# Performance work log

Hardware: AMD Instinct MI355X
Metric: run time of the kernel (lower is better)

## Reference

```python
import jax, jax.numpy as jnp
import numpy as np

D = 256  # channel dim and CBP output dim


def setup_inputs() -> dict:
    key = jax.random.key(0)
    ks = jax.random.split(key, 14)
    B, C, H, W = 32, 256, 56, 56
    attr_num = 400
    inp = {}
    inp["entity_feature"] = jax.random.normal(ks[0], (B, C, H, W), jnp.float32)
    inp["attr_one_hot"] = jax.random.uniform(ks[1], (B, attr_num), jnp.float32)
    # textual_emb: Linear(attr_num, 256)
    inp["W_emb"] = jax.random.normal(ks[2], (D, attr_num), jnp.float32) * 0.02
    inp["b_emb"] = jnp.zeros((D,), jnp.float32)
    # conv: Conv2d(256,256,1)
    inp["conv_w"] = jax.random.normal(ks[3], (D, D), jnp.float32) * 0.02
    inp["conv_b"] = jnp.zeros((D,), jnp.float32)
    # mcb_conv1_attr: Conv2d(256,32,1)
    inp["conv1_w"] = jax.random.normal(ks[4], (32, D), jnp.float32) * 0.05
    inp["conv1_b"] = jnp.zeros((32,), jnp.float32)
    # mcb_conv2_attr: Conv2d(32,1,1)
    inp["conv2_w"] = jax.random.normal(ks[5], (1, 32), jnp.float32) * 0.1
    inp["conv2_b"] = jnp.zeros((1,), jnp.float32)
    # CompactBilinearPooling count-sketch tables (fixed random at init)
    inp["h1"] = jax.random.randint(ks[6], (D,), 0, D, jnp.int32)
    inp["h2"] = jax.random.randint(ks[7], (D,), 0, D, jnp.int32)
    inp["s1"] = (jax.random.randint(ks[8], (D,), 0, 2, jnp.int32) * 2 - 1).astype(jnp.float32)
    inp["s2"] = (jax.random.randint(ks[9], (D,), 0, 2, jnp.int32) * 2 - 1).astype(jnp.float32)
    return inp


def _sketch_matrix(h, s):
    # sparse count-sketch projection as dense [C_in, D] matrix: P[i, h[i]] = s[i]
    return jnp.zeros((D, D), jnp.float32).at[jnp.arange(D), h].add(s)


def reference(entity_feature, attr_one_hot, W_emb, b_emb, conv_w, conv_b,
              conv1_w, conv1_b, conv2_w, conv2_b, h1, h2, s1, s2):
    feature = jax.nn.relu(entity_feature)                      # [B,256,H,W]
    # textual embedding + spatially-constant 1x1 conv (identical math to
    # expanding then convolving, since the expanded tensor is constant over HxW)
    t = attr_one_hot @ W_emb.T + b_emb                         # [B,256]
    a = t @ conv_w.T + conv_b                                  # [B,256]

    # Compact Bilinear Pooling (count sketch -> FFT -> elementwise mul -> iFFT)
    P1 = _sketch_matrix(h1, s1)
    P2 = _sketch_matrix(h2, s2)
    sk1 = a @ P1                                               # [B,256], spatially constant
    sk2 = jnp.einsum('bchw,cd->bdhw', feature, P2)             # [B,256,H,W]
    fft1 = jnp.fft.rfft(sk1, n=D, axis=1)[:, :, None, None]    # [B,129,1,1]
    fft2 = jnp.fft.rfft(sk2, n=D, axis=1)                      # [B,129,H,W]
    mcb = jnp.fft.irfft(fft1 * fft2, n=D, axis=1)              # [B,256,H,W]

    # gating chain: conv1x1 -> relu -> conv1x1 -> sigmoid
    x = jax.nn.relu(jnp.einsum('bchw,oc->bohw', mcb, conv1_w) + conv1_b[None, :, None, None])
    attr_map = jax.nn.sigmoid(jnp.einsum('bchw,oc->bohw', x, conv2_w) + conv2_b[None, :, None, None])  # [B,1,H,W]
    attr_feature = attr_map * entity_feature                   # [B,256,H,W]
    return attr_map, attr_feature
```

## Files before the change

kernel.cpp:

```cpp
#include <hip/hip_runtime.h>

#define Dq    256
#define ATTR  400
#define HW    3136
#define NB    32
#define PXT   64
#define NTILE 49

typedef __attribute__((ext_vector_type(8))) short bf16x8;
typedef __attribute__((ext_vector_type(4))) float f32x4;

__device__ __forceinline__ unsigned short f2bf(float f) {
  unsigned int x = __float_as_uint(f);
  return (unsigned short)((x + 0x7FFFu + ((x >> 16) & 1u)) >> 16);
}

__device__ __forceinline__ void g2lds16(const float* g, float* l) {
  __builtin_amdgcn_global_load_lds(
      (const __attribute__((address_space(1))) unsigned int*)g,
      (__attribute__((address_space(3))) unsigned int*)l,
      16, 0, 0);
}

__global__ __launch_bounds__(256) void k_sk1(
    const float* __restrict__ oh, const float* __restrict__ W_emb,
    const float* __restrict__ b_emb, const float* __restrict__ conv_w,
    const float* __restrict__ conv_b, const int* __restrict__ h1,
    const float* __restrict__ s1, float* __restrict__ sk1_out) {
  __shared__ float ohs[ATTR];
  __shared__ float ts[Dq];
  __shared__ float sk[Dq];
  const int b = blockIdx.x, tid = threadIdx.x;
  for (int j = tid; j < ATTR; j += 256) ohs[j] = oh[b * ATTR + j];
  sk[tid] = 0.f;
  __syncthreads();
  float acc = b_emb[tid];
  const float* wr = W_emb + tid * ATTR;
  for (int j = 0; j < ATTR; ++j) acc = fmaf(ohs[j], wr[j], acc);
  ts[tid] = acc;
  __syncthreads();
  float a = conv_b[tid];
  const float* cr = conv_w + tid * Dq;
  for (int k = 0; k < Dq; ++k) a = fmaf(ts[k], cr[k], a);
  atomicAdd(&sk[h1[tid]], a * s1[tid]);
  __syncthreads();
  sk1_out[b * Dq + tid] = sk[tid];
}

__global__ __launch_bounds__(256) void k_G(
    const float* __restrict__ sk1, const float* __restrict__ conv1_w,
    const int* __restrict__ h2, const float* __restrict__ s2,
    unsigned short* __restrict__ Abuf) {
  __shared__ float sks[Dq];
  __shared__ float w1[Dq];
  __shared__ float Tl[Dq];
  const int b = blockIdx.x >> 5, o = blockIdx.x & 31, c = threadIdx.x;
  sks[c] = sk1[b * Dq + c];
  w1[c]  = conv1_w[o * Dq + c];
  __syncthreads();
  float t = 0.f;
  for (int d = 0; d < Dq; ++d) t = fmaf(w1[d], sks[(d - c) & 255], t);
  Tl[c] = t;
  __syncthreads();
  const float g = s2[c] * Tl[h2[c]];
  const int frag = (o >> 4) * 8 + (c >> 5);
  const int lane = (o & 15) | (((c >> 3) & 3) << 4);
  Abuf[(((size_t)b * 16 + frag) * 64 + lane) * 8 + (c & 7)] = f2bf(g);
}

__global__ __launch_bounds__(256) void k_tile(
    const float* __restrict__ ent,
    const unsigned short* __restrict__ Abuf,
    const float* __restrict__ c1b, const float* __restrict__ c2w,
    const float* __restrict__ c2b,
    float* __restrict__ out)
{
  __shared__ float tile[Dq * PXT];
  __shared__ float s_lds[PXT];
  const int b = blockIdx.y;
  const int px_base = blockIdx.x * PXT;
  const int t = threadIdx.x;
  const int w = t >> 6, l = t & 63;

  const float* eb = ent + (size_t)b * Dq * HW + px_base;

#pragma unroll
  for (int i = 0; i < 16; ++i) {
    const int cb = w * 64 + i * 4;
    const float* src = eb + (size_t)(cb + (l >> 4)) * HW + 4 * (l & 15);
    g2lds16(src, &tile[cb * PXT]);
  }
  asm volatile("s_waitcnt vmcnt(0)");
  __syncthreads();

  const int n = l & 15, kg = l >> 4;
  const unsigned short* Ab = Abuf + ((size_t)b * 16 * 64 + l) * 8;

  f32x4 acc0 = {0.f, 0.f, 0.f, 0.f}, acc1 = {0.f, 0.f, 0.f, 0.f};
#pragma unroll
  for (int ks = 0; ks < 8; ++ks) {
    bf16x8 bv;
#pragma unroll
    for (int j = 0; j < 8; ++j) {
      const float fv = tile[(ks * 32 + kg * 8 + j) * PXT + w * 16 + n];
      bv[j] = (short)f2bf(fmaxf(fv, 0.f));
    }
    bf16x8 a0 = *reinterpret_cast<const bf16x8*>(Ab + (size_t)(0 * 8 + ks) * 64 * 8);
    bf16x8 a1 = *reinterpret_cast<const bf16x8*>(Ab + (size_t)(1 * 8 + ks) * 64 * 8);
    acc0 = __builtin_amdgcn_mfma_f32_16x16x32_bf16(a0, bv, acc0, 0, 0, 0);
    acc1 = __builtin_amdgcn_mfma_f32_16x16x32_bf16(a1, bv, acc1, 0, 0, 0);
  }

  const float4 b1a = reinterpret_cast<const float4*>(c1b)[kg];
  const float4 b1b = reinterpret_cast<const float4*>(c1b)[kg + 4];
  const float4 w2a = reinterpret_cast<const float4*>(c2w)[kg];
  const float4 w2b = reinterpret_cast<const float4*>(c2w)[kg + 4];
  float z = 0.f;
  z = fmaf(w2a.x, fmaxf(acc0[0] + b1a.x, 0.f), z);
  z = fmaf(w2a.y, fmaxf(acc0[1] + b1a.y, 0.f), z);
  z = fmaf(w2a.z, fmaxf(acc0[2] + b1a.z, 0.f), z);
  z = fmaf(w2a.w, fmaxf(acc0[3] + b1a.w, 0.f), z);
  z = fmaf(w2b.x, fmaxf(acc1[0] + b1b.x, 0.f), z);
  z = fmaf(w2b.y, fmaxf(acc1[1] + b1b.y, 0.f), z);
  z = fmaf(w2b.z, fmaxf(acc1[2] + b1b.z, 0.f), z);
  z = fmaf(w2b.w, fmaxf(acc1[3] + b1b.w, 0.f), z);
  z += __shfl_xor(z, 16);
  z += __shfl_xor(z, 32);
  const float s = 1.f / (1.f + __expf(-(z + c2b[0])));
  if (l < 16) {
    out[(size_t)b * HW + px_base + w * 16 + l] = s;
    s_lds[w * 16 + l] = s;
  }
  __syncthreads();

  const f32x4 s4v = *reinterpret_cast<const f32x4*>(&s_lds[(t & 15) * 4]);
  float* fb = out + (size_t)NB * HW + (size_t)b * Dq * HW + px_base;
#pragma unroll
  for (int k = 0; k < 16; ++k) {
    const int c = k * 16 + (t >> 4);
    f32x4 e = *reinterpret_cast<const f32x4*>(&tile[c * PXT + (t & 15) * 4]);
    *reinterpret_cast<f32x4*>(fb + (size_t)c * HW + (t & 15) * 4) = e * s4v;
  }
}

extern "C" void kernel_launch(void* const* d_in, const int* in_sizes, int n_in,
                              void* d_out, int out_size, void* d_ws, size_t ws_size,
                              hipStream_t stream) {
  const float* ent    = (const float*)d_in[0];
  const float* oh     = (const float*)d_in[1];
  const float* W_emb  = (const float*)d_in[2];
  const float* b_emb  = (const float*)d_in[3];
  const float* conv_w = (const float*)d_in[4];
  const float* conv_b = (const float*)d_in[5];
  const float* c1w    = (const float*)d_in[6];
  const float* c1b    = (const float*)d_in[7];
  const float* c2w    = (const float*)d_in[8];
  const float* c2b    = (const float*)d_in[9];
  const int*   h1     = (const int*)d_in[10];
  const int*   h2     = (const int*)d_in[11];
  const float* s1     = (const float*)d_in[12];
  const float* s2     = (const float*)d_in[13];

  float* ws  = (float*)d_ws;
  float* sk1 = ws;
  unsigned short* Abuf = (unsigned short*)(ws + NB * Dq);

  hipLaunchKernelGGL(k_sk1, dim3(NB), dim3(256), 0, stream,
                     oh, W_emb, b_emb, conv_w, conv_b, h1, s1, sk1);
  hipLaunchKernelGGL(k_G, dim3(NB * 32), dim3(256), 0, stream,
                     sk1, c1w, h2, s2, Abuf);
  hipLaunchKernelGGL(k_tile, dim3(NTILE, NB), dim3(256), 0, stream,
                     ent, Abuf, c1b, c2w, c2b, (float*)d_out);
}
```

Measured before the change: 73.22 us.

## Make tile kernel persistent with double-buffered LDS prefetch of entity tiles

The tile kernel becomes persistent: 256 blocks loop over all 1568 batch×pixel tiles instead of one tile per block. Each block keeps two 64 KB LDS tile buffers and issues global-to-LDS loads for the next tile before computing the current one, synchronising with vmcnt waits and raw barriers. The aim is to hide the streaming load latency behind the MFMA gating and output writes, and to cut block launch overhead. In exchange, the 128 KB LDS footprint limits each CU to one 4-wave block, so much less latency is hidden by occupancy. The vmcnt waits also cover outstanding stores, which can stall the loop.

```diff
diff --git a/kernel.cpp b/kernel.cpp
--- a/kernel.cpp
+++ b/kernel.cpp
@@ -5,7 +5,7 @@
 #define HW    3136
 #define NB    32
 #define PXT   64
-#define NTILE 49
+#define NTT   (NB * 49)
 
 typedef __attribute__((ext_vector_type(8))) short bf16x8;
 typedef __attribute__((ext_vector_type(4))) float f32x4;
@@ -75,71 +75,94 @@
     const float* __restrict__ c2b,
     float* __restrict__ out)
 {
-  __shared__ float tile[Dq * PXT];
+  __shared__ float tile[2][Dq * PXT];
   __shared__ float s_lds[PXT];
-  const int b = blockIdx.y;
-  const int px_base = blockIdx.x * PXT;
   const int t = threadIdx.x;
   const int w = t >> 6, l = t & 63;
-
-  const float* eb = ent + (size_t)b * Dq * HW + px_base;
-
-#pragma unroll
-  for (int i = 0; i < 16; ++i) {
-    const int cb = w * 64 + i * 4;
-    const float* src = eb + (size_t)(cb + (l >> 4)) * HW + 4 * (l & 15);
-    g2lds16(src, &tile[cb * PXT]);
-  }
-  asm volatile("s_waitcnt vmcnt(0)");
-  __syncthreads();
-
   const int n = l & 15, kg = l >> 4;
-  const unsigned short* Ab = Abuf + ((size_t)b * 16 * 64 + l) * 8;
-
-  f32x4 acc0 = {0.f, 0.f, 0.f, 0.f}, acc1 = {0.f, 0.f, 0.f, 0.f};
-#pragma unroll
-  for (int ks = 0; ks < 8; ++ks) {
-    bf16x8 bv;
-#pragma unroll
-    for (int j = 0; j < 8; ++j) {
-      const float fv = tile[(ks * 32 + kg * 8 + j) * PXT + w * 16 + n];
-      bv[j] = (short)f2bf(fmaxf(fv, 0.f));
-    }
-    bf16x8 a0 = *reinterpret_cast<const bf16x8*>(Ab + (size_t)(0 * 8 + ks) * 64 * 8);
-    bf16x8 a1 = *reinterpret_cast<const bf16x8*>(Ab + (size_t)(1 * 8 + ks) * 64 * 8);
-    acc0 = __builtin_amdgcn_mfma_f32_16x16x32_bf16(a0, bv, acc0, 0, 0, 0);
-    acc1 = __builtin_amdgcn_mfma_f32_16x16x32_bf16(a1, bv, acc1, 0, 0, 0);
-  }
 
   const float4 b1a = reinterpret_cast<const float4*>(c1b)[kg];
   const float4 b1b = reinterpret_cast<const float4*>(c1b)[kg + 4];
   const float4 w2a = reinterpret_cast<const float4*>(c2w)[kg];
   const float4 w2b = reinterpret_cast<const float4*>(c2w)[kg + 4];
-  float z = 0.f;
-  z = fmaf(w2a.x, fmaxf(acc0[0] + b1a.x, 0.f), z);
-  z = fmaf(w2a.y, fmaxf(acc0[1] + b1a.y, 0.f), z);
-  z = fmaf(w2a.z, fmaxf(acc0[2] + b1a.z, 0.f), z);
-  z = fmaf(w2a.w, fmaxf(acc0[3] + b1a.w, 0.f), z);
-  z = fmaf(w2b.x, fmaxf(acc1[0] + b1b.x, 0.f), z);
-  z = fmaf(w2b.y, fmaxf(acc1[1] + b1b.y, 0.f), z);
-  z = fmaf(w2b.z, fmaxf(acc1[2] + b1b.z, 0.f), z);
-  z = fmaf(w2b.w, fmaxf(acc1[3] + b1b.w, 0.f), z);
-  z += __shfl_xor(z, 16);
-  z += __shfl_xor(z, 32);
-  const float s = 1.f / (1.f + __expf(-(z + c2b[0])));
-  if (l < 16) {
-    out[(size_t)b * HW + px_base + w * 16 + l] = s;
-    s_lds[w * 16 + l] = s;
+  const float c2b0 = c2b[0];
+
+  {
+    const int ti = blockIdx.x;
+    const int bb = ti / 49, pxt = ti - bb * 49;
+    const float* eb = ent + (size_t)bb * Dq * HW + pxt * PXT;
+#pragma unroll
+    for (int i = 0; i < 16; ++i) {
+      const int cb = w * 64 + i * 4;
+      g2lds16(eb + (size_t)(cb + (l >> 4)) * HW + 4 * (l & 15), &tile[0][cb * PXT]);
+    }
   }
-  __syncthreads();
 
-  const f32x4 s4v = *reinterpret_cast<const f32x4*>(&s_lds[(t & 15) * 4]);
-  float* fb = out + (size_t)NB * HW + (size_t)b * Dq * HW + px_base;
+  int buf = 0;
+  for (int ti = blockIdx.x; ti < NTT; ti += 256, buf ^= 1) {
+    const int nxt = ti + 256;
+    if (nxt < NTT) {
+      const int bb = nxt / 49, pxt = nxt - bb * 49;
+      const float* eb = ent + (size_t)bb * Dq * HW + pxt * PXT;
 #pragma unroll
-  for (int k = 0; k < 16; ++k) {
-    const int c = k * 16 + (t >> 4);
-    f32x4 e = *reinterpret_cast<const f32x4*>(&tile[c * PXT + (t & 15) * 4]);
-    *reinterpret_cast<f32x4*>(fb + (size_t)c * HW + (t & 15) * 4) = e * s4v;
+      for (int i = 0; i < 16; ++i) {
+        const int cb = w * 64 + i * 4;
+        g2lds16(eb + (size_t)(cb + (l >> 4)) * HW + 4 * (l & 15), &tile[buf ^ 1][cb * PXT]);
+      }
+    }
+    asm volatile("s_waitcnt vmcnt(16)" ::: "memory");
+    __builtin_amdgcn_sched_barrier(0);
+    __builtin_amdgcn_s_barrier();
+
+    const int bb = ti / 49, pxt = ti - bb * 49;
+    const int px_base = pxt * PXT;
+    const float* tb = &tile[buf][0];
+
+    const unsigned short* Ab = Abuf + ((size_t)bb * 16 * 64 + l) * 8;
+    f32x4 acc0 = {0.f, 0.f, 0.f, 0.f}, acc1 = {0.f, 0.f, 0.f, 0.f};
+#pragma unroll
+    for (int ks = 0; ks < 8; ++ks) {
+      bf16x8 bv;
+#pragma unroll
+      for (int j = 0; j < 8; ++j) {
+        const float fv = tb[(ks * 32 + kg * 8 + j) * PXT + w * 16 + n];
+        bv[j] = (short)f2bf(fmaxf(fv, 0.f));
+      }
+      bf16x8 a0 = *reinterpret_cast<const bf16x8*>(Ab + (size_t)(0 * 8 + ks) * 64 * 8);
+      bf16x8 a1 = *reinterpret_cast<const bf16x8*>(Ab + (size_t)(1 * 8 + ks) * 64 * 8);
+      acc0 = __builtin_amdgcn_mfma_f32_16x16x32_bf16(a0, bv, acc0, 0, 0, 0);
+      acc1 = __builtin_amdgcn_mfma_f32_16x16x32_bf16(a1, bv, acc1, 0, 0, 0);
+    }
+
+    float z = 0.f;
+    z = fmaf(w2a.x, fmaxf(acc0[0] + b1a.x, 0.f), z);
+    z = fmaf(w2a.y, fmaxf(acc0[1] + b1a.y, 0.f), z);
+    z = fmaf(w2a.z, fmaxf(acc0[2] + b1a.z, 0.f), z);
+    z = fmaf(w2a.w, fmaxf(acc0[3] + b1a.w, 0.f), z);
+    z = fmaf(w2b.x, fmaxf(acc1[0] + b1b.x, 0.f), z);
+    z = fmaf(w2b.y, fmaxf(acc1[1] + b1b.y, 0.f), z);
+    z = fmaf(w2b.z, fmaxf(acc1[2] + b1b.z, 0.f), z);
+    z = fmaf(w2b.w, fmaxf(acc1[3] + b1b.w, 0.f), z);
+    z += __shfl_xor(z, 16);
+    z += __shfl_xor(z, 32);
+    const float s = 1.f / (1.f + __expf(-(z + c2b0)));
+    if (l < 16) {
+      out[(size_t)bb * HW + px_base + w * 16 + l] = s;
+      s_lds[w * 16 + l] = s;
+    }
+    asm volatile("s_waitcnt lgkmcnt(0)" ::: "memory");
+    __builtin_amdgcn_s_barrier();
+
+    const f32x4 s4v = *reinterpret_cast<const f32x4*>(&s_lds[(t & 15) * 4]);
+    float* fb = out + (size_t)NB * HW + (size_t)bb * Dq * HW + px_base;
+#pragma unroll
+    for (int k = 0; k < 16; ++k) {
+      const int c = k * 16 + (t >> 4);
+      f32x4 e = *reinterpret_cast<const f32x4*>(&tb[c * PXT + (t & 15) * 4]);
+      *reinterpret_cast<f32x4*>(fb + (size_t)c * HW + (t & 15) * 4) = e * s4v;
+    }
+    asm volatile("s_waitcnt lgkmcnt(0)" ::: "memory");
+    __builtin_amdgcn_s_barrier();
   }
 }
 
@@ -169,6 +192,6 @@
                      oh, W_emb, b_emb, conv_w, conv_b, h1, s1, sk1);
   hipLaunchKernelGGL(k_G, dim3(NB * 32), dim3(256), 0, stream,
                      sk1, c1w, h2, s2, Abuf);
-  hipLaunchKernelGGL(k_tile, dim3(NTILE, NB), dim3(256), 0, stream,
+  hipLaunchKernelGGL(k_tile, dim3(256), dim3(256), 0, stream,
                      ent, Abuf, c1b, c2w, c2b, (float*)d_out);
 }
```

Result: no change. 73.69 us (+0.6%).

## Double-buffer channel slabs over wider pixel tiles and re-read input for output

Applied to the files above, without the earlier changes.

The per-tile kernel now covers 224 pixels per block instead of 64. It streams the 256 input channels in 32-channel slabs through two LDS buffers, so global loads overlap with the MFMA gating compute. The bf16 A fragments are hoisted into registers once per block. The gated output pass now re-reads the entity tensor from global memory instead of from LDS, which saves LDS space but adds a second read of the large input that depends on cache hits. The grid also shrinks from 1568 to 448 blocks, which changes the load balance across CUs.

```diff
diff --git a/kernel.cpp b/kernel.cpp
--- a/kernel.cpp
+++ b/kernel.cpp
@@ -4,8 +4,9 @@
 #define ATTR  400
 #define HW    3136
 #define NB    32
-#define PXT   64
-#define NTILE 49
+#define P     224
+#define NTX   14
+#define SLABB 28672
 
 typedef __attribute__((ext_vector_type(8))) short bf16x8;
 typedef __attribute__((ext_vector_type(4))) float f32x4;
@@ -68,78 +69,121 @@
   Abuf[(((size_t)b * 16 + frag) * 64 + lane) * 8 + (c & 7)] = f2bf(g);
 }
 
-__global__ __launch_bounds__(256) void k_tile(
+__global__ __launch_bounds__(256) void k_big(
     const float* __restrict__ ent,
     const unsigned short* __restrict__ Abuf,
     const float* __restrict__ c1b, const float* __restrict__ c2w,
     const float* __restrict__ c2b,
     float* __restrict__ out)
 {
-  __shared__ float tile[Dq * PXT];
-  __shared__ float s_lds[PXT];
-  const int b = blockIdx.y;
-  const int px_base = blockIdx.x * PXT;
+  __shared__ float buf[2][SLABB / 4];
+  __shared__ float s_lds[P];
   const int t = threadIdx.x;
   const int w = t >> 6, l = t & 63;
+  const int n = l & 15, kg = l >> 4;
+  const int b = blockIdx.x / NTX, tix = blockIdx.x % NTX;
+  const int px_base = tix * P;
 
   const float* eb = ent + (size_t)b * Dq * HW + px_base;
 
-#pragma unroll
-  for (int i = 0; i < 16; ++i) {
-    const int cb = w * 64 + i * 4;
-    const float* src = eb + (size_t)(cb + (l >> 4)) * HW + 4 * (l & 15);
-    g2lds16(src, &tile[cb * PXT]);
-  }
-  asm volatile("s_waitcnt vmcnt(0)");
-  __syncthreads();
-
-  const int n = l & 15, kg = l >> 4;
   const unsigned short* Ab = Abuf + ((size_t)b * 16 * 64 + l) * 8;
-
-  f32x4 acc0 = {0.f, 0.f, 0.f, 0.f}, acc1 = {0.f, 0.f, 0.f, 0.f};
-#pragma unroll
-  for (int ks = 0; ks < 8; ++ks) {
-    bf16x8 bv;
-#pragma unroll
-    for (int j = 0; j < 8; ++j) {
-      const float fv = tile[(ks * 32 + kg * 8 + j) * PXT + w * 16 + n];
-      bv[j] = (short)f2bf(fmaxf(fv, 0.f));
-    }
-    bf16x8 a0 = *reinterpret_cast<const bf16x8*>(Ab + (size_t)(0 * 8 + ks) * 64 * 8);
-    bf16x8 a1 = *reinterpret_cast<const bf16x8*>(Ab + (size_t)(1 * 8 + ks) * 64 * 8);
-    acc0 = __builtin_amdgcn_mfma_f32_16x16x32_bf16(a0, bv, acc0, 0, 0, 0);
-    acc1 = __builtin_amdgcn_mfma_f32_16x16x32_bf16(a1, bv, acc1, 0, 0, 0);
+  bf16x8 A0[8], A1[8];
+#pragma unroll
+  for (int k = 0; k < 8; ++k) {
+    A0[k] = *reinterpret_cast<const bf16x8*>(Ab + (size_t)(0 * 8 + k) * 64 * 8);
+    A1[k] = *reinterpret_cast<const bf16x8*>(Ab + (size_t)(1 * 8 + k) * 64 * 8);
   }
 
   const float4 b1a = reinterpret_cast<const float4*>(c1b)[kg];
   const float4 b1b = reinterpret_cast<const float4*>(c1b)[kg + 4];
   const float4 w2a = reinterpret_cast<const float4*>(c2w)[kg];
   const float4 w2b = reinterpret_cast<const float4*>(c2w)[kg + 4];
-  float z = 0.f;
-  z = fmaf(w2a.x, fmaxf(acc0[0] + b1a.x, 0.f), z);
-  z = fmaf(w2a.y, fmaxf(acc0[1] + b1a.y, 0.f), z);
-  z = fmaf(w2a.z, fmaxf(acc0[2] + b1a.z, 0.f), z);
-  z = fmaf(w2a.w, fmaxf(acc0[3] + b1a.w, 0.f), z);
-  z = fmaf(w2b.x, fmaxf(acc1[0] + b1b.x, 0.f), z);
-  z = fmaf(w2b.y, fmaxf(acc1[1] + b1b.y, 0.f), z);
-  z = fmaf(w2b.z, fmaxf(acc1[2] + b1b.z, 0.f), z);
-  z = fmaf(w2b.w, fmaxf(acc1[3] + b1b.w, 0.f), z);
-  z += __shfl_xor(z, 16);
-  z += __shfl_xor(z, 32);
-  const float s = 1.f / (1.f + __expf(-(z + c2b[0])));
-  if (l < 16) {
-    out[(size_t)b * HW + px_base + w * 16 + l] = s;
-    s_lds[w * 16 + l] = s;
-  }
-  __syncthreads();
-
-  const f32x4 s4v = *reinterpret_cast<const f32x4*>(&s_lds[(t & 15) * 4]);
-  float* fb = out + (size_t)NB * HW + (size_t)b * Dq * HW + px_base;
-#pragma unroll
-  for (int k = 0; k < 16; ++k) {
-    const int c = k * 16 + (t >> 4);
-    f32x4 e = *reinterpret_cast<const f32x4*>(&tile[c * PXT + (t & 15) * 4]);
-    *reinterpret_cast<f32x4*>(fb + (size_t)c * HW + (t & 15) * 4) = e * s4v;
+  const float c2b0 = c2b[0];
+
+#define STAGE(sl, bs)                                                          \
+  {                                                                            \
+    const float* sb = eb + (size_t)(sl) * 32 * HW;                             \
+    _Pragma("unroll")                                                          \
+    for (int i = 0; i < 7; ++i) {                                              \
+      const int dbase = i * 4096 + w * 1024;                                   \
+      const int dl = dbase + l * 16;                                           \
+      const int cc = dl / 896;                                                 \
+      const int off = dl - cc * 896;                                           \
+      g2lds16(sb + (size_t)cc * HW + (off >> 2), &buf[bs][dbase >> 2]);        \
+    }                                                                          \
+  }
+
+  f32x4 acc[4][2];
+#pragma unroll
+  for (int ii = 0; ii < 4; ++ii) { acc[ii][0] = f32x4{0,0,0,0}; acc[ii][1] = f32x4{0,0,0,0}; }
+
+  STAGE(0, 0);
+  int cur = 0;
+#pragma unroll
+  for (int k = 0; k < 8; ++k) {
+    if (k < 7) {
+      STAGE(k + 1, cur ^ 1);
+      asm volatile("s_waitcnt vmcnt(7)" ::: "memory");
+    } else {
+      asm volatile("s_waitcnt vmcnt(0)" ::: "memory");
+    }
+    __builtin_amdgcn_sched_barrier(0);
+    __builtin_amdgcn_s_barrier();
+
+    const float* tb = &buf[cur][0];
+#pragma unroll
+    for (int ii = 0; ii < 4; ++ii) {
+      const int ti = w + 4 * ii;
+      if (ti < NTX) {
+        bf16x8 bv;
+#pragma unroll
+        for (int j = 0; j < 8; ++j) {
+          const float fv = tb[(kg * 8 + j) * P + ti * 16 + n];
+          bv[j] = (short)f2bf(fmaxf(fv, 0.f));
+        }
+        acc[ii][0] = __builtin_amdgcn_mfma_f32_16x16x32_bf16(A0[k], bv, acc[ii][0], 0, 0, 0);
+        acc[ii][1] = __builtin_amdgcn_mfma_f32_16x16x32_bf16(A1[k], bv, acc[ii][1], 0, 0, 0);
+      }
+    }
+    __builtin_amdgcn_s_barrier();
+    cur ^= 1;
+  }
+
+#pragma unroll
+  for (int ii = 0; ii < 4; ++ii) {
+    const int ti = w + 4 * ii;
+    if (ti < NTX) {
+      float z = 0.f;
+      z = fmaf(w2a.x, fmaxf(acc[ii][0][0] + b1a.x, 0.f), z);
+      z = fmaf(w2a.y, fmaxf(acc[ii][0][1] + b1a.y, 0.f), z);
+      z = fmaf(w2a.z, fmaxf(acc[ii][0][2] + b1a.z, 0.f), z);
+      z = fmaf(w2a.w, fmaxf(acc[ii][0][3] + b1a.w, 0.f), z);
+      z = fmaf(w2b.x, fmaxf(acc[ii][1][0] + b1b.x, 0.f), z);
+      z = fmaf(w2b.y, fmaxf(acc[ii][1][1] + b1b.y, 0.f), z);
+      z = fmaf(w2b.z, fmaxf(acc[ii][1][2] + b1b.z, 0.f), z);
+      z = fmaf(w2b.w, fmaxf(acc[ii][1][3] + b1b.w, 0.f), z);
+      z += __shfl_xor(z, 16);
+      z += __shfl_xor(z, 32);
+      const float s = 1.f / (1.f + __expf(-(z + c2b0)));
+      if (kg == 0) {
+        out[(size_t)b * HW + px_base + ti * 16 + n] = s;
+        s_lds[ti * 16 + n] = s;
+      }
+    }
+  }
+  __syncthreads();
+
+  const f32x4* eb4 = reinterpret_cast<const f32x4*>(eb);
+  f32x4* fb4 = reinterpret_cast<f32x4*>(out + (size_t)NB * HW + (size_t)b * Dq * HW + px_base);
+  const f32x4* sl4 = reinterpret_cast<const f32x4*>(s_lds);
+#pragma unroll 4
+  for (int k2 = 0; k2 < 56; ++k2) {
+    const int u = k2 * 256 + t;
+    const int c = u / 56;
+    const int q = u - c * 56;
+    f32x4 e = eb4[c * 784 + q];
+    f32x4 r = e * sl4[q];
+    fb4[c * 784 + q] = r;
   }
 }
 
@@ -169,6 +213,6 @@
                      oh, W_emb, b_emb, conv_w, conv_b, h1, s1, sk1);
   hipLaunchKernelGGL(k_G, dim3(NB * 32), dim3(256), 0, stream,
                      sk1, c1w, h2, s2, Abuf);
-  hipLaunchKernelGGL(k_tile, dim3(NTILE, NB), dim3(256), 0, stream,
+  hipLaunchKernelGGL(k_big, dim3(NB * NTX), dim3(256), 0, stream,
                      ent, Abuf, c1b, c2w, c2b, (float*)d_out);
 }
```

After: 94.33 us. 28.8% more time.

## Split gating-map computation and elementwise multiply into separate kernels

Applied to the files above, without the earlier changes.

The fused tile kernel used to compute the attention map and then write attr_feature from the LDS-resident tile. This change splits that into a map-only kernel and a separate streaming multiply kernel that re-reads entity_feature and the map and writes with nontemporal stores. It aims to shorten the map kernel and get a fully coalesced, high-occupancy multiply pass. The cost is re-reading about 100MB of input from HBM and an extra launch.

```diff
diff --git a/kernel.cpp b/kernel.cpp
--- a/kernel.cpp
+++ b/kernel.cpp
@@ -68,7 +68,7 @@
   Abuf[(((size_t)b * 16 + frag) * 64 + lane) * 8 + (c & 7)] = f2bf(g);
 }
 
-__global__ __launch_bounds__(256) void k_tile(
+__global__ __launch_bounds__(256) void k_map(
     const float* __restrict__ ent,
     const unsigned short* __restrict__ Abuf,
     const float* __restrict__ c1b, const float* __restrict__ c2w,
@@ -76,7 +76,6 @@
     float* __restrict__ out)
 {
   __shared__ float tile[Dq * PXT];
-  __shared__ float s_lds[PXT];
   const int b = blockIdx.y;
   const int px_base = blockIdx.x * PXT;
   const int t = threadIdx.x;
@@ -87,8 +86,7 @@
 #pragma unroll
   for (int i = 0; i < 16; ++i) {
     const int cb = w * 64 + i * 4;
-    const float* src = eb + (size_t)(cb + (l >> 4)) * HW + 4 * (l & 15);
-    g2lds16(src, &tile[cb * PXT]);
+    g2lds16(eb + (size_t)(cb + (l >> 4)) * HW + 4 * (l & 15), &tile[cb * PXT]);
   }
   asm volatile("s_waitcnt vmcnt(0)");
   __syncthreads();
@@ -127,19 +125,23 @@
   z += __shfl_xor(z, 16);
   z += __shfl_xor(z, 32);
   const float s = 1.f / (1.f + __expf(-(z + c2b[0])));
-  if (l < 16) {
-    out[(size_t)b * HW + px_base + w * 16 + l] = s;
-    s_lds[w * 16 + l] = s;
-  }
-  __syncthreads();
+  if (l < 16) out[(size_t)b * HW + px_base + w * 16 + l] = s;
+}
 
-  const f32x4 s4v = *reinterpret_cast<const f32x4*>(&s_lds[(t & 15) * 4]);
-  float* fb = out + (size_t)NB * HW + (size_t)b * Dq * HW + px_base;
+__global__ __launch_bounds__(256) void k_mul(
+    const float* __restrict__ ent, float* __restrict__ out) {
+  const f32x4* e4 = reinterpret_cast<const f32x4*>(ent);
+  const f32x4* m4 = reinterpret_cast<const f32x4*>(out);
+  f32x4* f4 = reinterpret_cast<f32x4*>(out + (size_t)NB * HW);
+  const int base = blockIdx.x * 3584 + threadIdx.x;
 #pragma unroll
-  for (int k = 0; k < 16; ++k) {
-    const int c = k * 16 + (t >> 4);
-    f32x4 e = *reinterpret_cast<const f32x4*>(&tile[c * PXT + (t & 15) * 4]);
-    *reinterpret_cast<f32x4*>(fb + (size_t)c * HW + (t & 15) * 4) = e * s4v;
+  for (int i = 0; i < 14; ++i) {
+    const int f = base + i * 256;
+    const int r = f / 784;
+    const int q = f - r * 784;
+    const int b = r >> 8;
+    f32x4 v = e4[f] * m4[b * 784 + q];
+    __builtin_nontemporal_store(v, &f4[f]);
   }
 }
 
@@ -169,6 +171,8 @@
                      oh, W_emb, b_emb, conv_w, conv_b, h1, s1, sk1);
   hipLaunchKernelGGL(k_G, dim3(NB * 32), dim3(256), 0, stream,
                      sk1, c1w, h2, s2, Abuf);
-  hipLaunchKernelGGL(k_tile, dim3(NTILE, NB), dim3(256), 0, stream,
+  hipLaunchKernelGGL(k_map, dim3(NTILE, NB), dim3(256), 0, stream,
                      ent, Abuf, c1b, c2w, c2b, (float*)d_out);
+  hipLaunchKernelGGL(k_mul, dim3(1792), dim3(256), 0, stream,
+                     ent, (float*)d_out);
 }
```

Measured after the change: 87.43 us. +19.4%, slower.
